# Performance work log

Hardware: AMD Instinct MI355X
Metric: run time of the kernel (lower is better)

## Reference

```python
import jax, jax.numpy as jnp
import numpy as np

N, E, C = 50000, 10000, 500
NNZ = 400000
IN_DIM, EDGE_DIM, NODE_DIM, COMP_DIM = 128, 128, 128, 128


def _glorot(key, shape):
    fan = shape[0] + shape[1]
    return jax.random.normal(key, shape, jnp.float32) * (2.0 / fan) ** 0.5


def _seg_mean(vals, idx, num):
    # mean aggregation over segments (scatter-add + count normalize)
    s = jax.ops.segment_sum(vals, idx, num_segments=num)
    cnt = jax.ops.segment_sum(jnp.ones((idx.shape[0], 1), vals.dtype), idx, num_segments=num)
    return s / jnp.maximum(cnt, 1.0)


def _prelu(v, a):
    return jnp.where(v >= 0, v, a * v)


def _conv(x, ni, ei, ec_e, ec_c, nc_n, nc_c, n_nodes, n_edges, n_comps,
          Wne, Wen, Wec, Wnc, a):
    # node -> hyperedge message passing
    e = _seg_mean((x @ Wne)[ni], ei, n_edges)            # [E, edge_dim]
    e_act = _prelu(e, a)
    # hyperedge -> node
    n = _seg_mean((e_act @ Wen)[ei], ni, n_nodes)        # [N, node_dim]
    # edge -> component and node -> component
    c = _seg_mean((e_act @ Wec)[ec_e], ec_c, n_comps) + \
        _seg_mean((x @ Wnc)[nc_n], nc_c, n_comps)        # [C, comp_dim]
    return n, e, c


def setup_inputs() -> dict:
    key = jax.random.key(0)
    ks = jax.random.split(key, 16)
    x = jax.random.normal(ks[0], (N, IN_DIM), jnp.float32)
    hyperedge_index = jnp.stack([
        jax.random.randint(ks[1], (NNZ,), 0, N),
        jax.random.randint(ks[2], (NNZ,), 0, E),
    ])
    hyperedge_component_index = jnp.stack([
        jnp.arange(E), jax.random.randint(ks[3], (E,), 0, C)])
    node_component_index = jnp.stack([
        jnp.arange(N), jax.random.randint(ks[4], (N,), 0, C)])
    return dict(
        x=x,
        hyperedge_index=hyperedge_index,
        hyperedge_component_index=hyperedge_component_index,
        node_component_index=node_component_index,
        num_nodes=N, num_edges=E, num_components=C,
        W_ne0=_glorot(ks[5], (IN_DIM, EDGE_DIM)),
        W_en0=_glorot(ks[6], (EDGE_DIM, NODE_DIM)),
        W_ec0=_glorot(ks[7], (EDGE_DIM, COMP_DIM)),
        W_nc0=_glorot(ks[8], (IN_DIM, COMP_DIM)),
        W_ne1=_glorot(ks[9], (NODE_DIM, EDGE_DIM)),
        W_en1=_glorot(ks[10], (EDGE_DIM, NODE_DIM)),
        W_ec1=_glorot(ks[11], (EDGE_DIM, COMP_DIM)),
        W_nc1=_glorot(ks[12], (NODE_DIM, COMP_DIM)),
        prelu_a=jnp.array(0.25, jnp.float32),
    )


def reference(x, hyperedge_index, hyperedge_component_index, node_component_index,
              num_nodes, num_edges, num_components,
              W_ne0, W_en0, W_ec0, W_nc0, W_ne1, W_en1, W_ec1, W_nc1, prelu_a):
    ni, ei = hyperedge_index[0], hyperedge_index[1]
    ec_e, ec_c = hyperedge_component_index[0], hyperedge_component_index[1]
    nc_n, nc_c = node_component_index[0], node_component_index[1]
    layers = [(W_ne0, W_en0, W_ec0, W_nc0), (W_ne1, W_en1, W_ec1, W_nc1)]
    e_out = c_out = None
    for Wne, Wen, Wec, Wnc in layers:
        n_out, e_out, c_out = _conv(x, ni, ei, ec_e, ec_c, nc_n, nc_c,
                                    num_nodes, num_edges, num_components,
                                    Wne, Wen, Wec, Wnc, prelu_a)
        x = _prelu(n_out, prelu_a)  # HyperEncoder applies act between/after layers
    return (x, e_out, c_out)
```

## Files before the change

kernel.cpp:

```cpp
#include <hip/hip_runtime.h>
#include <stdint.h>

typedef unsigned int u32;
typedef _Float16 f16;
typedef f16 half8 __attribute__((ext_vector_type(8)));
typedef float f32x4 __attribute__((ext_vector_type(4)));
#define TS 4096
#define KB2 256
#define CH 2048

__device__ __forceinline__ float bflo(u32 u) { return __uint_as_float(u << 16); }
__device__ __forceinline__ float bfhi(u32 u) { return __uint_as_float(u & 0xffff0000u); }
__device__ __forceinline__ u32 f2bf(float x) {
    u32 u = __float_as_uint(x);
    return (u + 0x7fffu + ((u >> 16) & 1u)) >> 16;
}
__device__ __forceinline__ u32 pack2(float a, float b) { return f2bf(a) | (f2bf(b) << 16); }

__device__ __forceinline__ int bstart2(int b, int total) {
    return (int)(((unsigned long long)b * (u32)total + KB2 - 1) / KB2);
}

__device__ __forceinline__ int blk_exscan(int v, int& total) {
    __shared__ int ws[5];
    int t = threadIdx.x, lane = t & 63, w = t >> 6;
    int inc = v;
    for (int d = 1; d < 64; d <<= 1) { int u = __shfl_up(inc, d, 64); if (lane >= d) inc += u; }
    __syncthreads();
    if (lane == 63) ws[w] = inc;
    __syncthreads();
    if (t == 0) { int acc = 0; for (int i = 0; i < 4; ++i) { int x = ws[i]; ws[i] = acc; acc += x; } ws[4] = acc; }
    __syncthreads();
    total = ws[4];
    return ws[w] + (inc - v);
}

__global__ void k_wprep(const float* __restrict__ W0, const float* __restrict__ W1,
                        const float* __restrict__ W2, const float* __restrict__ W3,
                        const float* __restrict__ W4, const float* __restrict__ W5,
                        f16* __restrict__ out) {
    int gid = blockIdx.x * 256 + threadIdx.x;
    if (gid >= 6 * 2048) return;
    int m = gid >> 11;
    int rem = gid & 2047;
    int c = rem >> 4;
    int s = rem & 15;
    const float* W = (m == 0) ? W0 : (m == 1) ? W1 : (m == 2) ? W2 :
                     (m == 3) ? W3 : (m == 4) ? W4 : W5;
    int khi = ((s & 7) ^ (c & 7)) | (s & 8);
    int k0 = khi << 3;
    union { f16 h[8]; uint4 v; } u;
#pragma unroll
    for (int j = 0; j < 8; ++j) u.h[j] = (f16)W[((k0 + j) << 7) + c];
    *(uint4*)(out + ((size_t)m << 14) + (c << 7) + (s << 3)) = u.v;
}

__global__ __launch_bounds__(256) void k_cvt_bhist(
        const float2* __restrict__ xin, u32* __restrict__ xout, int npairs,
        const int* __restrict__ ni, const int* __restrict__ ei,
        const int* __restrict__ nc_c, const int* __restrict__ ec_c,
        int* __restrict__ bcntE, int* __restrict__ bcntN,
        int* __restrict__ cnt_cn, int* __restrict__ cnt_ce,
        int nnz, int n, int e, int nbh) {
    int t = threadIdx.x;
    int b = blockIdx.x;
    if (b >= nbh) {
        int j = (b - nbh) * 256 + t;
        if (j < npairs) { float2 v = xin[j]; xout[j] = pack2(v.x, v.y); }
        return;
    }
    __shared__ int hE[KB2], hN[KB2];
    hE[t] = 0; hN[t] = 0;
    __syncthreads();
    int base = b * CH;
    int lim = base + CH; if (lim > nnz) lim = nnz;
    for (int i = base + t; i < lim; i += 256) {
        u32 v = (u32)ni[i], eg = (u32)ei[i];
        if (v >= (u32)n) v = 0;
        if (eg >= (u32)e) eg = 0;
        atomicAdd(&hE[(int)(((unsigned long long)eg * KB2) / (u32)e)], 1);
        atomicAdd(&hN[(int)(((unsigned long long)v  * KB2) / (u32)n)], 1);
    }
    __syncthreads();
    if (hE[t]) atomicAdd(&bcntE[t], hE[t]);
    if (hN[t]) atomicAdd(&bcntN[t], hN[t]);
    int gid = b * 256 + t, stride = nbh * 256;
    for (int j = gid; j < n + e; j += stride) {
        if (j < n) atomicAdd(&cnt_cn[nc_c[j]], 1);
        else       atomicAdd(&cnt_ce[ec_c[j - n]], 1);
    }
}

__global__ void k_cvt(const float2* __restrict__ in, u32* __restrict__ out, int npairs) {
    int j = blockIdx.x * blockDim.x + threadIdx.x;
    if (j < npairs) { float2 v = in[j]; out[j] = pack2(v.x, v.y); }
}

__global__ __launch_bounds__(256) void k_bscan(
        const int* __restrict__ bcntE, const int* __restrict__ bcntN,
        int* __restrict__ basesE, int* __restrict__ basesN,
        int* __restrict__ bcur_e, int* __restrict__ bcur_n,
        const int* __restrict__ cnt_cn, const int* __restrict__ cnt_ce,
        int* __restrict__ off_cn, int* __restrict__ off_ce,
        int* __restrict__ cur_cn, int* __restrict__ cur_ce, int c) {
    int t = threadIdx.x, tot;
    int v = bcntE[t];
    int ex = blk_exscan(v, tot);
    basesE[t] = ex; bcur_e[t] = ex;
    if (t == 0) basesE[KB2] = tot;
    v = bcntN[t];
    ex = blk_exscan(v, tot);
    basesN[t] = ex; bcur_n[t] = ex;
    if (t == 0) basesN[KB2] = tot;
    int i0 = 2 * t, i1 = 2 * t + 1;
    int v0 = (i0 < c) ? cnt_cn[i0] : 0;
    int v1 = (i1 < c) ? cnt_cn[i1] : 0;
    ex = blk_exscan(v0 + v1, tot);
    if (i0 < c) { off_cn[i0] = ex;      cur_cn[i0] = ex; }
    if (i1 < c) { off_cn[i1] = ex + v0; cur_cn[i1] = ex + v0; }
    if (t == 0) off_cn[c] = tot;
    v0 = (i0 < c) ? cnt_ce[i0] : 0;
    v1 = (i1 < c) ? cnt_ce[i1] : 0;
    ex = blk_exscan(v0 + v1, tot);
    if (i0 < c) { off_ce[i0] = ex;      cur_ce[i0] = ex; }
    if (i1 < c) { off_ce[i1] = ex + v0; cur_ce[i1] = ex + v0; }
    if (t == 0) off_ce[c] = tot;
}

__global__ __launch_bounds__(256) void k_part_a(
        const int* __restrict__ ni, const int* __restrict__ ei,
        int* __restrict__ bcur_e, int* __restrict__ bcur_n,
        u32* __restrict__ stg_e, u32* __restrict__ stg_n,
        const int* __restrict__ nc_n, const int* __restrict__ nc_c,
        const int* __restrict__ ec_e, const int* __restrict__ ec_c,
        int* __restrict__ cur_cn, int* __restrict__ cur_ce,
        int* __restrict__ csr_cn, int* __restrict__ csr_ce,
        int nnz, int n, int e) {
    __shared__ u32 pk[CH];
    __shared__ unsigned short bb[CH];
    __shared__ int hist[KB2];
    __shared__ int gb[KB2];
    int side = blockIdx.y;
    int base = blockIdx.x * CH;
    int cnt  = nnz - base; if (cnt > CH) cnt = CH;
    int t = threadIdx.x;
    for (int i = t; i < KB2; i += 256) hist[i] = 0;
    __syncthreads();
    u32 total = side ? (u32)n : (u32)e;
    for (int i = t; i < cnt; i += 256) {
        int v = ni[base + i], eg = ei[base + i];
        u32 key = side ? (u32)v : (u32)eg;
        u32 pay = side ? (u32)eg : (u32)v;
        if (key >= total) key = 0;
        u32 b = (u32)(((unsigned long long)key * KB2) / total);
        pk[i] = side ? (pay | (key << 14)) : (pay | (key << 16));
        bb[i] = (unsigned short)b;
        atomicAdd(&hist[b], 1);
    }
    __syncthreads();
    int* cursor = side ? bcur_n : bcur_e;
    u32* stg    = side ? stg_n  : stg_e;
    if (t < KB2) {
        int h = hist[t];
        gb[t] = h ? atomicAdd(&cursor[t], h) : 0;
        hist[t] = 0;
    }
    __syncthreads();
    for (int i = t; i < cnt; i += 256) {
        int b = bb[i];
        int r = atomicAdd(&hist[b], 1);
        stg[gb[b] + r] = pk[i];
    }
    int gid = blockIdx.x * 256 + t;
    int stride = gridDim.x * 256;
    if (side == 0) {
        for (int j = gid; j < e; j += stride) { int c = ec_c[j]; csr_ce[atomicAdd(&cur_ce[c], 1)] = ec_e[j]; }
    } else {
        for (int j = gid; j < n; j += stride) { int c = nc_c[j]; csr_cn[atomicAdd(&cur_cn[c], 1)] = nc_n[j]; }
    }
}

__global__ __launch_bounds__(256) void k_part_b2(
        const u32* __restrict__ stg_e, const u32* __restrict__ stg_n,
        const int* __restrict__ basesE, const int* __restrict__ basesN,
        int* __restrict__ off_e, int* __restrict__ off_n,
        int* __restrict__ csr_e, int* __restrict__ csr_n, int e, int n) {
    __shared__ int lcnt[256];
    int b = blockIdx.x, t = threadIdx.x;
    const u32* stg; const int* bases; int* off; int* csr; int total; int shift; u32 mask;
    if (b < KB2) { stg = stg_e; bases = basesE; off = off_e; csr = csr_e; total = e; shift = 16; mask = 0xFFFFu; }
    else { b -= KB2; stg = stg_n; bases = basesN; off = off_n; csr = csr_n; total = n; shift = 14; mask = 0x3FFFu; }
    int lo = bstart2(b, total), hi = bstart2(b + 1, total);
    int nid = hi - lo;
    int sbase = bases[b], send = bases[b + 1];
    lcnt[t] = 0;
    __syncthreads();
    for (int i = sbase + t; i < send; i += 256) {
        int key = (int)(stg[i] >> shift);
        atomicAdd(&lcnt[key - lo], 1);
    }
    __syncthreads();
    int cval = (t < nid) ? lcnt[t] : 0;
    int tot;
    int ex = blk_exscan(cval, tot);
    int cursor = sbase + ex;
    if (t < nid) { off[lo + t] = cursor; lcnt[t] = cursor; }
    if (t == 0 && hi == total) off[total] = send;
    __syncthreads();
    for (int i = sbase + t; i < send; i += 256) {
        u32 s = stg[i];
        int key = (int)(s >> shift);
        int pay = (int)(s & mask);
        int p = atomicAdd(&lcnt[key - lo], 1);
        csr[p] = pay;
    }
}

__global__ void k_hist_fb(const int* __restrict__ ni, const int* __restrict__ ei,
                          const int* __restrict__ nc_c, const int* __restrict__ ec_c,
                          int* __restrict__ deg_e, int* __restrict__ deg_n,
                          int* __restrict__ cnt_cn, int* __restrict__ cnt_ce,
                          int nnz, int n, int e) {
    int j = blockIdx.x * blockDim.x + threadIdx.x;
    if (j < nnz) {
        atomicAdd(&deg_e[ei[j]], 1);
        atomicAdd(&deg_n[ni[j]], 1);
    }
    if (j < n) atomicAdd(&cnt_cn[nc_c[j]], 1);
    if (j < e) atomicAdd(&cnt_ce[ec_c[j]], 1);
}

__device__ __forceinline__ void scan_sel(int b, int t0, int t01, int t012,
        const int* c0, int* o0, int* u0, int n0,
        const int* c1, int* o1, int* u1, int n1,
        const int* c2, int* o2, int* u2, int n2,
        const int* c3, int* o3, int* u3, int n3,
        const int*& cnt, int*& off, int*& cur, int& n, int& tile) {
    if (b < t0)        { cnt = c0; off = o0; cur = u0; n = n0; tile = b; }
    else if (b < t01)  { cnt = c1; off = o1; cur = u1; n = n1; tile = b - t0; }
    else if (b < t012) { cnt = c2; off = o2; cur = u2; n = n2; tile = b - t01; }
    else               { cnt = c3; off = o3; cur = u3; n = n3; tile = b - t012; }
}

__global__ void k_scan_p1(const int* c0, int n0, const int* c1, int n1,
                          const int* c2, int n2, const int* c3, int n3,
                          int t0, int t01, int t012, int* __restrict__ tilesum) {
    __shared__ int ws[4];
    int b = blockIdx.x;
    const int* cnt; int* off; int* cur; int n; int tile;
    scan_sel(b, t0, t01, t012, c0, nullptr, nullptr, n0, c1, nullptr, nullptr, n1,
             c2, nullptr, nullptr, n2, c3, nullptr, nullptr, n3, cnt, off, cur, n, tile);
    int base = tile * TS + threadIdx.x * 16;
    int s = 0;
#pragma unroll
    for (int i = 0; i < 16; ++i) { int idx = base + i; if (idx < n) s += cnt[idx]; }
    for (int d = 32; d; d >>= 1) s += __shfl_xor(s, d, 64);
    int lane = threadIdx.x & 63, w = threadIdx.x >> 6;
    if (lane == 0) ws[w] = s;
    __syncthreads();
    if (threadIdx.x == 0) tilesum[b] = ws[0] + ws[1] + ws[2] + ws[3];
}

__global__ void k_scan_p2(const int* __restrict__ tilesum, int* __restrict__ tilebase,
                          int t0, int t01, int t012, int t0123,
                          int* o0, int n0, int* o1, int n1, int* o2, int n2, int* o3, int n3) {
    if (threadIdx.x != 0 || blockIdx.x != 0) return;
    int carry = 0;
    for (int b = 0;    b < t0;    ++b) { tilebase[b] = carry; carry += tilesum[b]; } o0[n0] = carry;
    carry = 0;
    for (int b = t0;   b < t01;   ++b) { tilebase[b] = carry; carry += tilesum[b]; } o1[n1] = carry;
    carry = 0;
    for (int b = t01;  b < t012;  ++b) { tilebase[b] = carry; carry += tilesum[b]; } o2[n2] = carry;
    carry = 0;
    for (int b = t012; b < t0123; ++b) { tilebase[b] = carry; carry += tilesum[b]; } o3[n3] = carry;
}

__global__ void k_scan_p3(const int* c0, int* o0, int* u0, int n0,
                          const int* c1, int* o1, int* u1, int n1,
                          const int* c2, int* o2, int* u2, int n2,
                          const int* c3, int* o3, int* u3, int n3,
                          int t0, int t01, int t012, const int* __restrict__ tilebase) {
    __shared__ int wsum[4];
    int b = blockIdx.x;
    const int* cnt; int* off; int* cur; int n; int tile;
    scan_sel(b, t0, t01, t012, c0, o0, u0, n0, c1, o1, u1, n1,
             c2, o2, u2, n2, c3, o3, u3, n3, cnt, off, cur, n, tile);
    int lane = threadIdx.x & 63, w = threadIdx.x >> 6;
    int base = tile * TS + threadIdx.x * 16;
    int vals[16];
    int s = 0;
#pragma unroll
    for (int i = 0; i < 16; ++i) { int idx = base + i; int v = (idx < n) ? cnt[idx] : 0; vals[i] = v; s += v; }
    int inc = s;
    for (int d = 1; d < 64; d <<= 1) { int u = __shfl_up(inc, d, 64); if (lane >= d) inc += u; }
    if (lane == 63) wsum[w] = inc;
    __syncthreads();
    if (threadIdx.x == 0) {
        int acc = tilebase[b];
        for (int i = 0; i < 4; ++i) { int t = wsum[i]; wsum[i] = acc; acc += t; }
    }
    __syncthreads();
    int ex = wsum[w] + (inc - s);
#pragma unroll
    for (int i = 0; i < 16; ++i) {
        int idx = base + i;
        if (idx < n) { off[idx] = ex; cur[idx] = ex; }
        ex += vals[i];
    }
}

__global__ void k_scatter(const int* __restrict__ ni, const int* __restrict__ ei,
                          const int* __restrict__ nc_n, const int* __restrict__ nc_c,
                          const int* __restrict__ ec_e, const int* __restrict__ ec_c,
                          int* __restrict__ cur_e, int* __restrict__ cur_n,
                          int* __restrict__ cur_cn, int* __restrict__ cur_ce,
                          int* __restrict__ csr_e, int* __restrict__ csr_n,
                          int* __restrict__ csr_cn, int* __restrict__ csr_ce,
                          int nnz, int n, int e) {
    int j = blockIdx.x * blockDim.x + threadIdx.x;
    if (j < nnz) {
        int v = ni[j], eg = ei[j];
        csr_e[atomicAdd(&cur_e[eg], 1)] = v;
        csr_n[atomicAdd(&cur_n[v], 1)] = eg;
    }
    if (j < n) { int c = nc_c[j]; csr_cn[atomicAdd(&cur_cn[c], 1)] = nc_n[j]; }
    if (j < e) { int c = ec_c[j]; csr_ce[atomicAdd(&cur_ce[c], 1)] = ec_e[j]; }
}

__device__ __forceinline__ void agg4_body(const u32* __restrict__ in,
                                          const int* __restrict__ items,
                                          const int* __restrict__ off,
                                          float* __restrict__ out_f32,
                                          u32* __restrict__ out_bf,
                                          int nseg, int nrows, int do_prelu,
                                          const float* __restrict__ alpha_p, int seg) {
    int lane = threadIdx.x & 63;
    int rs = lane >> 4;
    int cc = lane & 15;
    if (seg >= nseg) return;
    int s0 = off[seg], s1 = off[seg + 1];
    const uint4* rows = (const uint4*)in;
    float a[8];
#pragma unroll
    for (int i = 0; i < 8; ++i) a[i] = 0.f;
    int base = s0;
    for (; base + 8 <= s1; base += 8) {
        u32 r0 = (u32)items[base + rs];
        u32 r1 = (u32)items[base + 4 + rs];
        r0 = (r0 < (u32)nrows) ? r0 : 0u;
        r1 = (r1 < (u32)nrows) ? r1 : 0u;
        uint4 v0 = rows[(size_t)r0 * 16 + cc];
        uint4 v1 = rows[(size_t)r1 * 16 + cc];
        a[0] += bflo(v0.x); a[1] += bfhi(v0.x); a[2] += bflo(v0.y); a[3] += bfhi(v0.y);
        a[4] += bflo(v0.z); a[5] += bfhi(v0.z); a[6] += bflo(v0.w); a[7] += bfhi(v0.w);
        a[0] += bflo(v1.x); a[1] += bfhi(v1.x); a[2] += bflo(v1.y); a[3] += bfhi(v1.y);
        a[4] += bflo(v1.z); a[5] += bfhi(v1.z); a[6] += bflo(v1.w); a[7] += bfhi(v1.w);
    }
    int idx = base + rs;
    if (idx < s1) {
        u32 r = (u32)items[idx]; r = (r < (u32)nrows) ? r : 0u;
        uint4 v = rows[(size_t)r * 16 + cc];
        a[0] += bflo(v.x); a[1] += bfhi(v.x); a[2] += bflo(v.y); a[3] += bfhi(v.y);
        a[4] += bflo(v.z); a[5] += bfhi(v.z); a[6] += bflo(v.w); a[7] += bfhi(v.w);
    }
    idx += 4;
    if (idx < s1) {
        u32 r = (u32)items[idx]; r = (r < (u32)nrows) ? r : 0u;
        uint4 v = rows[(size_t)r * 16 + cc];
        a[0] += bflo(v.x); a[1] += bfhi(v.x); a[2] += bflo(v.y); a[3] += bfhi(v.y);
        a[4] += bflo(v.z); a[5] += bfhi(v.z); a[6] += bflo(v.w); a[7] += bfhi(v.w);
    }
#pragma unroll
    for (int i = 0; i < 8; ++i) {
        a[i] += __shfl_xor(a[i], 16, 64);
        a[i] += __shfl_xor(a[i], 32, 64);
    }
    float inv = 1.f / fmaxf((float)(s1 - s0), 1.f);
#pragma unroll
    for (int i = 0; i < 8; ++i) a[i] *= inv;
    if (do_prelu) {
        float al = *alpha_p;
#pragma unroll
        for (int i = 0; i < 8; ++i) a[i] = (a[i] >= 0.f) ? a[i] : al * a[i];
    }
    if (rs == 0) {
        if (out_f32) {
            float* o = out_f32 + ((size_t)seg << 7) + cc * 8;
            *(float4*)o       = make_float4(a[0], a[1], a[2], a[3]);
            *(float4*)(o + 4) = make_float4(a[4], a[5], a[6], a[7]);
        }
        if (out_bf) {
            uint4 pk;
            pk.x = pack2(a[0], a[1]); pk.y = pack2(a[2], a[3]);
            pk.z = pack2(a[4], a[5]); pk.w = pack2(a[6], a[7]);
            *(uint4*)(out_bf + ((size_t)seg << 6) + cc * 4) = pk;
        }
    }
}

__global__ void k_agg4(const u32* __restrict__ in, const int* __restrict__ items,
                       const int* __restrict__ off, float* __restrict__ out_f32,
                       u32* __restrict__ out_bf,
                       int nseg, int nrows, int do_prelu, const float* __restrict__ alpha_p) {
    int seg = blockIdx.x * (blockDim.x >> 6) + (threadIdx.x >> 6);
    agg4_body(in, items, off, out_f32, out_bf, nseg, nrows, do_prelu, alpha_p, seg);
}

__global__ void k_agg_final(
        const u32* __restrict__ ybf, const int* __restrict__ csr_n, const int* __restrict__ off_n,
        float* __restrict__ out_x, int n, int e,
        const u32* __restrict__ eactbf, const int* __restrict__ csr_ce, const int* __restrict__ off_ce,
        float* __restrict__ ca_e,
        const u32* __restrict__ x1bf, const int* __restrict__ csr_cn, const int* __restrict__ off_cn,
        float* __restrict__ ca_n,
        int c, int nblkN, int ncb, const float* __restrict__ alpha_p) {
    int b = blockIdx.x;
    int wv = threadIdx.x >> 6;
    if (b < nblkN) {
        agg4_body(ybf, csr_n, off_n, out_x, nullptr, n, e, 1, alpha_p, b * 4 + wv);
    } else if (b < nblkN + ncb) {
        agg4_body(eactbf, csr_ce, off_ce, ca_e, nullptr, c, e, 0, nullptr, (b - nblkN) * 4 + wv);
    } else {
        agg4_body(x1bf, csr_cn, off_cn, ca_n, nullptr, c, n, 0, nullptr, (b - nblkN - ncb) * 4 + wv);
    }
}

__global__ __launch_bounds__(256) void k_mlp_mfma(
        const float* __restrict__ A,
        const f16* __restrict__ W1t, const f16* __restrict__ W2t,
        float* __restrict__ out_raw, u32* __restrict__ out_actbf,
        u32* __restrict__ out_ybf, int M, const float* __restrict__ alpha_p) {
    __shared__ f16 As[32 * 128];
    __shared__ f16 Wt[128 * 128];
    int t = threadIdx.x;
    int rb = blockIdx.x * 32;
    float al = *alpha_p;
    {
        const uint4* src = (const uint4*)W1t;
        uint4* dst = (uint4*)Wt;
        for (int i = t; i < 2048; i += 256) dst[i] = src[i];
    }
    for (int i = t; i < 32 * 32; i += 256) {
        int r = i >> 5, dc = i & 31;
        int row = rb + r;
        float4 v = make_float4(0.f, 0.f, 0.f, 0.f);
        if (row < M) v = *(const float4*)(A + ((size_t)row << 7) + dc * 4);
        f16* p = (f16*)((char*)As + (r << 8) + ((dc << 3) ^ ((r & 7) << 4)));
        p[0] = (f16)v.x; p[1] = (f16)v.y; p[2] = (f16)v.z; p[3] = (f16)v.w;
    }
    __syncthreads();

    int lane = t & 63, wv = t >> 6;
    int r0  = (wv >> 1) << 4;
    int ctb = (wv & 1) << 2;
    int frow = lane & 15;
    int fk = (lane >> 4) << 3;
    int rl0 = r0 + ((lane >> 4) << 2);
    int ar = r0 + frow;
    int asw = (ar & 7) << 4;

    f32x4 acc[4] = {{0.f,0.f,0.f,0.f},{0.f,0.f,0.f,0.f},{0.f,0.f,0.f,0.f},{0.f,0.f,0.f,0.f}};
#pragma unroll
    for (int ks = 0; ks < 4; ++ks) {
        int kb2 = (ks * 32 + fk) << 1;
        half8 a = *(const half8*)((const char*)As + (ar << 8) + (kb2 ^ asw));
#pragma unroll
        for (int j = 0; j < 4; ++j) {
            int c = ((ctb + j) << 4) + frow;
            half8 b = *(const half8*)((const char*)Wt + (c << 8) + (kb2 ^ ((c & 7) << 4)));
            acc[j] = __builtin_amdgcn_mfma_f32_16x16x32_f16(a, b, acc[j], 0, 0, 0);
        }
    }
    __syncthreads();
    {
        const uint4* src = (const uint4*)W2t;
        uint4* dst = (uint4*)Wt;
        for (int i = t; i < 2048; i += 256) dst[i] = src[i];
    }
#pragma unroll
    for (int j = 0; j < 4; ++j) {
        int c = ((ctb + j) << 4) + frow;
#pragma unroll
        for (int rg = 0; rg < 4; ++rg) {
            int rl = rl0 + rg;
            int row = rb + rl;
            float ev = acc[j][rg];
            if (out_raw != nullptr && row < M) out_raw[((size_t)row << 7) + c] = ev;
            float av = (ev >= 0.f) ? ev : al * ev;
            float po = __shfl_xor(av, 1, 64);
            if (out_actbf != nullptr && (frow & 1) == 0 && row < M)
                out_actbf[((size_t)row << 6) + (c >> 1)] = pack2(av, po);
            *(f16*)((char*)As + (rl << 8) + (((c << 1)) ^ ((rl & 7) << 4))) = (f16)av;
        }
    }
    __syncthreads();
    f32x4 acc2[4] = {{0.f,0.f,0.f,0.f},{0.f,0.f,0.f,0.f},{0.f,0.f,0.f,0.f},{0.f,0.f,0.f,0.f}};
#pragma unroll
    for (int ks = 0; ks < 4; ++ks) {
        int kb2 = (ks * 32 + fk) << 1;
        half8 a = *(const half8*)((const char*)As + (ar << 8) + (kb2 ^ asw));
#pragma unroll
        for (int j = 0; j < 4; ++j) {
            int c = ((ctb + j) << 4) + frow;
            half8 b = *(const half8*)((const char*)Wt + (c << 8) + (kb2 ^ ((c & 7) << 4)));
            acc2[j] = __builtin_amdgcn_mfma_f32_16x16x32_f16(a, b, acc2[j], 0, 0, 0);
        }
    }
#pragma unroll
    for (int j = 0; j < 4; ++j) {
        int c = ((ctb + j) << 4) + frow;
#pragma unroll
        for (int rg = 0; rg < 4; ++rg) {
            int rl = rl0 + rg;
            int row = rb + rl;
            float yv = acc2[j][rg];
            float po = __shfl_xor(yv, 1, 64);
            if ((frow & 1) == 0 && row < M)
                out_ybf[((size_t)row << 6) + (c >> 1)] = pack2(yv, po);
        }
    }
}

__global__ __launch_bounds__(256) void k_gemm_mfma(
        const float* __restrict__ A1, const f16* __restrict__ W1t,
        const float* __restrict__ A2, const f16* __restrict__ W2t,
        float* __restrict__ out, int M) {
    __shared__ f16 Asd[2][32 * 128];
    __shared__ f16 Wt[128 * 128];
    int t = threadIdx.x;
    int rb = blockIdx.x * 32;
    {
        const uint4* src = (const uint4*)W1t;
        uint4* dst = (uint4*)Wt;
        for (int i = t; i < 2048; i += 256) dst[i] = src[i];
    }
    for (int p = 0; p < 2; ++p) {
        const float* Ap = p ? A2 : A1;
        for (int i = t; i < 32 * 32; i += 256) {
            int r = i >> 5, dc = i & 31;
            int row = rb + r;
            float4 v = make_float4(0.f, 0.f, 0.f, 0.f);
            if (row < M) v = *(const float4*)(Ap + ((size_t)row << 7) + dc * 4);
            f16* q = (f16*)((char*)Asd[p] + (r << 8) + ((dc << 3) ^ ((r & 7) << 4)));
            q[0] = (f16)v.x; q[1] = (f16)v.y; q[2] = (f16)v.z; q[3] = (f16)v.w;
        }
    }
    __syncthreads();

    int lane = t & 63, wv = t >> 6;
    int r0  = (wv >> 1) << 4;
    int ctb = (wv & 1) << 2;
    int frow = lane & 15;
    int fk = (lane >> 4) << 3;
    int rl0 = r0 + ((lane >> 4) << 2);
    int ar = r0 + frow;
    int asw = (ar & 7) << 4;

    f32x4 acc[4] = {{0.f,0.f,0.f,0.f},{0.f,0.f,0.f,0.f},{0.f,0.f,0.f,0.f},{0.f,0.f,0.f,0.f}};
#pragma unroll
    for (int ks = 0; ks < 4; ++ks) {
        int kb2 = (ks * 32 + fk) << 1;
        half8 a = *(const half8*)((const char*)Asd[0] + (ar << 8) + (kb2 ^ asw));
#pragma unroll
        for (int j = 0; j < 4; ++j) {
            int c = ((ctb + j) << 4) + frow;
            half8 b = *(const half8*)((const char*)Wt + (c << 8) + (kb2 ^ ((c & 7) << 4)));
            acc[j] = __builtin_amdgcn_mfma_f32_16x16x32_f16(a, b, acc[j], 0, 0, 0);
        }
    }
    __syncthreads();
    {
        const uint4* src = (const uint4*)W2t;
        uint4* dst = (uint4*)Wt;
        for (int i = t; i < 2048; i += 256) dst[i] = src[i];
    }
    __syncthreads();
#pragma unroll
    for (int ks = 0; ks < 4; ++ks) {
        int kb2 = (ks * 32 + fk) << 1;
        half8 a = *(const half8*)((const char*)Asd[1] + (ar << 8) + (kb2 ^ asw));
#pragma unroll
        for (int j = 0; j < 4; ++j) {
            int c = ((ctb + j) << 4) + frow;
            half8 b = *(const half8*)((const char*)Wt + (c << 8) + (kb2 ^ ((c & 7) << 4)));
            acc[j] = __builtin_amdgcn_mfma_f32_16x16x32_f16(a, b, acc[j], 0, 0, 0);
        }
    }
#pragma unroll
    for (int j = 0; j < 4; ++j) {
        int c = ((ctb + j) << 4) + frow;
#pragma unroll
        for (int rg = 0; rg < 4; ++rg) {
            int row = rb + rl0 + rg;
            if (row < M) out[((size_t)row << 7) + c] = acc[j][rg];
        }
    }
}

extern "C" void kernel_launch(void* const* d_in, const int* in_sizes, int n_in,
                              void* d_out, int out_size, void* d_ws, size_t ws_size,
                              hipStream_t stream) {
    const int N   = in_sizes[0] / 128;
    const int NNZ = in_sizes[1] / 2;
    const int E   = in_sizes[2] / 2;
    const int C   = 500;

    const float* x0 = (const float*)d_in[0];
    const int* ni   = (const int*)d_in[1];
    const int* ei   = ni + NNZ;
    const int* ec_e = (const int*)d_in[2];
    const int* ec_c = ec_e + E;
    const int* nc_n = (const int*)d_in[3];
    const int* nc_c = nc_n + N;
    const float* Wne0 = (const float*)d_in[7];
    const float* Wen0 = (const float*)d_in[8];
    const float* Wne1 = (const float*)d_in[11];
    const float* Wen1 = (const float*)d_in[12];
    const float* Wec1 = (const float*)d_in[13];
    const float* Wnc1 = (const float*)d_in[14];
    const float* alpha = (const float*)d_in[15];

    float* out_x = (float*)d_out;
    float* out_e = out_x + (size_t)N * 128;
    float* out_c = out_e + (size_t)E * 128;

    char* w = (char*)d_ws;
    auto alloc = [&](size_t bytes) { char* p = w; w += (bytes + 255) & ~(size_t)255; return p; };
    int* zgrp   = (int*)alloc((size_t)(2 * KB2 + 2 * C) * 4);
    int* bcntE  = zgrp;
    int* bcntN  = zgrp + KB2;
    int* cnt_cn = zgrp + 2 * KB2;
    int* cnt_ce = zgrp + 2 * KB2 + C;
    int* off_e  = (int*)alloc((size_t)(E + 1) * 4);
    int* off_n  = (int*)alloc((size_t)(N + 1) * 4);
    int* off_cn = (int*)alloc((size_t)(C + 1) * 4);
    int* off_ce = (int*)alloc((size_t)(C + 1) * 4);
    int* cur_cn = (int*)alloc((size_t)C * 4);
    int* cur_ce = (int*)alloc((size_t)C * 4);
    int* csr_e  = (int*)alloc((size_t)NNZ * 4);
    int* csr_n  = (int*)alloc((size_t)NNZ * 4);
    int* csr_cn = (int*)alloc((size_t)N * 4);
    int* csr_ce = (int*)alloc((size_t)E * 4);
    int* basesE = (int*)alloc((size_t)(KB2 + 1) * 4);
    int* basesN = (int*)alloc((size_t)(KB2 + 1) * 4);
    int* bcur_e = (int*)alloc(KB2 * 4);
    int* bcur_n = (int*)alloc(KB2 * 4);
    u32* stg_e  = (u32*)alloc((size_t)NNZ * 4);
    u32* stg_n  = (u32*)alloc((size_t)NNZ * 4);
    u32* xbf    = (u32*)alloc((size_t)N * 64 * 4);
    u32* x1bf   = (u32*)alloc((size_t)N * 64 * 4);
    u32* ybf    = (u32*)alloc((size_t)E * 64 * 4);
    u32* eactbf = (u32*)alloc((size_t)E * 64 * 4);
    float* xa   = (float*)alloc((size_t)E * 128 * 4);
    float* ca_e = (float*)alloc((size_t)C * 128 * 4);
    float* ca_n = (float*)alloc((size_t)C * 128 * 4);
    f16* wt6    = (f16*)alloc((size_t)6 * 16384 * 2);
    int* deg_e    = (int*)alloc((size_t)E * 4);
    int* deg_n    = (int*)alloc((size_t)N * 4);
    int* cur_e    = (int*)alloc((size_t)E * 4);
    int* cur_n    = (int*)alloc((size_t)N * 4);
    int* tilesum  = (int*)alloc(64 * 4);
    int* tilebase = (int*)alloc(64 * 4);

    const int th = 256;
    const int npairs = N * 64;
    const int nbh = (NNZ + CH - 1) / CH;

    hipMemsetAsync(zgrp, 0, (size_t)(2 * KB2 + 2 * C) * 4, stream);
    k_wprep<<<48, 256, 0, stream>>>(Wne0, Wen0, Wne1, Wen1, Wec1, Wnc1, wt6);

    bool binned = (E <= 16384) && (N <= 65536) && (E >= KB2) && (N >= KB2) &&
                  ((N + KB2 - 1) / KB2 <= 256) && (C <= 512);
    if (binned) {
        const int nkc = (npairs + th - 1) / th;
        k_cvt_bhist<<<nbh + nkc, 256, 0, stream>>>((const float2*)x0, xbf, npairs,
                                                   ni, ei, nc_c, ec_c,
                                                   bcntE, bcntN, cnt_cn, cnt_ce, NNZ, N, E, nbh);
        k_bscan<<<1, 256, 0, stream>>>(bcntE, bcntN, basesE, basesN, bcur_e, bcur_n,
                                       cnt_cn, cnt_ce, off_cn, off_ce, cur_cn, cur_ce, C);
        {
            dim3 ga(nbh, 2);
            k_part_a<<<ga, 256, 0, stream>>>(ni, ei, bcur_e, bcur_n, stg_e, stg_n,
                                             nc_n, nc_c, ec_e, ec_c,
                                             cur_cn, cur_ce, csr_cn, csr_ce, NNZ, N, E);
        }
        k_part_b2<<<2 * KB2, 256, 0, stream>>>(stg_e, stg_n, basesE, basesN,
                                               off_e, off_n, csr_e, csr_n, E, N);
    } else {
        hipMemsetAsync(deg_e, 0, (size_t)E * 4, stream);
        hipMemsetAsync(deg_n, 0, (size_t)N * 4, stream);
        k_cvt<<<(npairs + th - 1) / th, th, 0, stream>>>((const float2*)x0, xbf, npairs);
        k_hist_fb<<<(NNZ > N + E ? NNZ : N + E) / th + 1, th, 0, stream>>>(
            ni, ei, nc_c, ec_c, deg_e, deg_n, cnt_cn, cnt_ce, NNZ, N, E);
        const int t0 = (E + TS - 1) / TS, t1 = (N + TS - 1) / TS;
        const int t2 = (C + TS - 1) / TS, t3 = (C + TS - 1) / TS;
        const int t01 = t0 + t1, t012 = t01 + t2, t0123 = t012 + t3;
        k_scan_p1<<<t0123, 256, 0, stream>>>(deg_e, E, deg_n, N, cnt_cn, C, cnt_ce, C,
                                             t0, t01, t012, tilesum);
        k_scan_p2<<<1, 64, 0, stream>>>(tilesum, tilebase, t0, t01, t012, t0123,
                                        off_e, E, off_n, N, off_cn, C, off_ce, C);
        k_scan_p3<<<t0123, 256, 0, stream>>>(deg_e, off_e, cur_e, E,
                                             deg_n, off_n, cur_n, N,
                                             cnt_cn, off_cn, cur_cn, C,
                                             cnt_ce, off_ce, cur_ce, C,
                                             t0, t01, t012, tilebase);
        k_scatter<<<(NNZ + th - 1) / th, th, 0, stream>>>(ni, ei, nc_n, nc_c, ec_e, ec_c,
                                                          cur_e, cur_n, cur_cn, cur_ce,
                                                          csr_e, csr_n, csr_cn, csr_ce, NNZ, N, E);
    }

    const int gmlp = (E + 31) / 32;
    k_agg4<<<(E + 3) / 4, 256, 0, stream>>>(xbf, csr_e, off_e, xa, nullptr, E, N, 0, alpha);
    k_mlp_mfma<<<gmlp, 256, 0, stream>>>(xa, wt6, wt6 + 16384, nullptr, nullptr, ybf, E, alpha);
    k_agg4<<<(N + 3) / 4, 256, 0, stream>>>(ybf, csr_n, off_n, nullptr, x1bf, N, E, 1, alpha);
    k_agg4<<<(E + 3) / 4, 256, 0, stream>>>(x1bf, csr_e, off_e, xa, nullptr, E, N, 0, alpha);
    k_mlp_mfma<<<gmlp, 256, 0, stream>>>(xa, wt6 + 2 * 16384, wt6 + 3 * 16384,
                                         out_e, eactbf, ybf, E, alpha);
    {
        const int nblkN = (N + 3) / 4;
        const int ncb   = (C + 3) / 4;
        k_agg_final<<<nblkN + 2 * ncb, 256, 0, stream>>>(
            ybf, csr_n, off_n, out_x, N, E,
            eactbf, csr_ce, off_ce, ca_e,
            x1bf,   csr_cn, off_cn, ca_n,
            C, nblkN, ncb, alpha);
    }
    k_gemm_mfma<<<(C + 31) / 32, 256, 0, stream>>>(ca_e, wt6 + 4 * 16384,
                                                   ca_n, wt6 + 5 * 16384, out_c, C);
}
```

Baseline: 268.9 us.

## Fuse edge aggregation into MLP kernel and merge front-end prep kernels

Edge-side segment-mean aggregation now runs inside the MFMA MLP kernel. It writes mean rows straight into shared memory as fp16 instead of going through an fp32 global buffer `xa`. The weight prep, conversion/histogram and block scan kernels are merged into a single launch, with the last-block ticket pattern doing the scan. The gather loop is also unrolled to 16 items. This removes several launches and a global round trip, at the cost of less parallelism in the aggregation phase (each wave handles 8 segments serially) and higher register and shared-memory pressure.

```diff
diff --git a/kernel.cpp b/kernel.cpp
--- a/kernel.cpp
+++ b/kernel.cpp
@@ -35,41 +35,144 @@
     return ws[w] + (inc - v);
 }
 
-__global__ void k_wprep(const float* __restrict__ W0, const float* __restrict__ W1,
-                        const float* __restrict__ W2, const float* __restrict__ W3,
-                        const float* __restrict__ W4, const float* __restrict__ W5,
-                        f16* __restrict__ out) {
-    int gid = blockIdx.x * 256 + threadIdx.x;
-    if (gid >= 6 * 2048) return;
-    int m = gid >> 11;
-    int rem = gid & 2047;
-    int c = rem >> 4;
-    int s = rem & 15;
-    const float* W = (m == 0) ? W0 : (m == 1) ? W1 : (m == 2) ? W2 :
-                     (m == 3) ? W3 : (m == 4) ? W4 : W5;
-    int khi = ((s & 7) ^ (c & 7)) | (s & 8);
-    int k0 = khi << 3;
-    union { f16 h[8]; uint4 v; } u;
-#pragma unroll
-    for (int j = 0; j < 8; ++j) u.h[j] = (f16)W[((k0 + j) << 7) + c];
-    *(uint4*)(out + ((size_t)m << 14) + (c << 7) + (s << 3)) = u.v;
-}
-
-__global__ __launch_bounds__(256) void k_cvt_bhist(
+#define ACC8(v) do { \
+    a[0] += bflo((v).x); a[1] += bfhi((v).x); a[2] += bflo((v).y); a[3] += bfhi((v).y); \
+    a[4] += bflo((v).z); a[5] += bfhi((v).z); a[6] += bflo((v).w); a[7] += bfhi((v).w); } while (0)
+
+__device__ __forceinline__ void seg_mean8(const u32* __restrict__ in,
+                                          const int* __restrict__ items,
+                                          const int* __restrict__ off,
+                                          int nseg, int nrows, int seg, float a[8]) {
+    int lane = threadIdx.x & 63;
+    int rs = lane >> 4;
+    int cc = lane & 15;
+#pragma unroll
+    for (int i = 0; i < 8; ++i) a[i] = 0.f;
+    int s0 = 0, s1 = 0;
+    if (seg < nseg) { s0 = off[seg]; s1 = off[seg + 1]; }
+    const uint4* rows = (const uint4*)in;
+    int base = s0;
+    for (; base + 16 <= s1; base += 16) {
+        u32 r0 = (u32)items[base + rs];
+        u32 r1 = (u32)items[base + 4 + rs];
+        u32 r2 = (u32)items[base + 8 + rs];
+        u32 r3 = (u32)items[base + 12 + rs];
+        r0 = (r0 < (u32)nrows) ? r0 : 0u;
+        r1 = (r1 < (u32)nrows) ? r1 : 0u;
+        r2 = (r2 < (u32)nrows) ? r2 : 0u;
+        r3 = (r3 < (u32)nrows) ? r3 : 0u;
+        uint4 v0 = rows[(size_t)r0 * 16 + cc];
+        uint4 v1 = rows[(size_t)r1 * 16 + cc];
+        uint4 v2 = rows[(size_t)r2 * 16 + cc];
+        uint4 v3 = rows[(size_t)r3 * 16 + cc];
+        ACC8(v0); ACC8(v1); ACC8(v2); ACC8(v3);
+    }
+    for (; base + 8 <= s1; base += 8) {
+        u32 r0 = (u32)items[base + rs];
+        u32 r1 = (u32)items[base + 4 + rs];
+        r0 = (r0 < (u32)nrows) ? r0 : 0u;
+        r1 = (r1 < (u32)nrows) ? r1 : 0u;
+        uint4 v0 = rows[(size_t)r0 * 16 + cc];
+        uint4 v1 = rows[(size_t)r1 * 16 + cc];
+        ACC8(v0); ACC8(v1);
+    }
+    int idx = base + rs;
+    if (idx < s1) {
+        u32 r = (u32)items[idx]; r = (r < (u32)nrows) ? r : 0u;
+        uint4 v = rows[(size_t)r * 16 + cc];
+        ACC8(v);
+    }
+    idx += 4;
+    if (idx < s1) {
+        u32 r = (u32)items[idx]; r = (r < (u32)nrows) ? r : 0u;
+        uint4 v = rows[(size_t)r * 16 + cc];
+        ACC8(v);
+    }
+#pragma unroll
+    for (int i = 0; i < 8; ++i) {
+        a[i] += __shfl_xor(a[i], 16, 64);
+        a[i] += __shfl_xor(a[i], 32, 64);
+    }
+    float inv = 1.f / fmaxf((float)(s1 - s0), 1.f);
+#pragma unroll
+    for (int i = 0; i < 8; ++i) a[i] *= inv;
+}
+
+__device__ __forceinline__ void agg4_body(const u32* __restrict__ in,
+                                          const int* __restrict__ items,
+                                          const int* __restrict__ off,
+                                          float* __restrict__ out_f32,
+                                          u32* __restrict__ out_bf,
+                                          int nseg, int nrows, int do_prelu,
+                                          const float* __restrict__ alpha_p, int seg) {
+    if (seg >= nseg) return;
+    int lane = threadIdx.x & 63;
+    int rs = lane >> 4;
+    int cc = lane & 15;
+    float a[8];
+    seg_mean8(in, items, off, nseg, nrows, seg, a);
+    if (do_prelu) {
+        float al = *alpha_p;
+#pragma unroll
+        for (int i = 0; i < 8; ++i) a[i] = (a[i] >= 0.f) ? a[i] : al * a[i];
+    }
+    if (rs == 0) {
+        if (out_f32) {
+            float* o = out_f32 + ((size_t)seg << 7) + cc * 8;
+            *(float4*)o       = make_float4(a[0], a[1], a[2], a[3]);
+            *(float4*)(o + 4) = make_float4(a[4], a[5], a[6], a[7]);
+        }
+        if (out_bf) {
+            uint4 pk;
+            pk.x = pack2(a[0], a[1]); pk.y = pack2(a[2], a[3]);
+            pk.z = pack2(a[4], a[5]); pk.w = pack2(a[6], a[7]);
+            *(uint4*)(out_bf + ((size_t)seg << 6) + cc * 4) = pk;
+        }
+    }
+}
+
+__global__ __launch_bounds__(256) void k_front(
         const float2* __restrict__ xin, u32* __restrict__ xout, int npairs,
         const int* __restrict__ ni, const int* __restrict__ ei,
         const int* __restrict__ nc_c, const int* __restrict__ ec_c,
         int* __restrict__ bcntE, int* __restrict__ bcntN,
         int* __restrict__ cnt_cn, int* __restrict__ cnt_ce,
-        int nnz, int n, int e, int nbh) {
+        int nnz, int n, int e, int nbh, int nkc,
+        int* __restrict__ ticket,
+        int* __restrict__ basesE, int* __restrict__ basesN,
+        int* __restrict__ bcur_e, int* __restrict__ bcur_n,
+        int* __restrict__ off_cn, int* __restrict__ off_ce,
+        int* __restrict__ cur_cn, int* __restrict__ cur_ce, int c,
+        const float* __restrict__ W0, const float* __restrict__ W1,
+        const float* __restrict__ W2, const float* __restrict__ W3,
+        const float* __restrict__ W4, const float* __restrict__ W5,
+        f16* __restrict__ wt6) {
     int t = threadIdx.x;
     int b = blockIdx.x;
+    if (b >= nbh + nkc) {
+        int gid = (b - nbh - nkc) * 256 + t;
+        if (gid >= 6 * 2048) return;
+        int m = gid >> 11;
+        int rem = gid & 2047;
+        int cq = rem >> 4;
+        int s = rem & 15;
+        const float* W = (m == 0) ? W0 : (m == 1) ? W1 : (m == 2) ? W2 :
+                         (m == 3) ? W3 : (m == 4) ? W4 : W5;
+        int khi = ((s & 7) ^ (cq & 7)) | (s & 8);
+        int k0 = khi << 3;
+        union { f16 h[8]; uint4 v; } u;
+#pragma unroll
+        for (int j = 0; j < 8; ++j) u.h[j] = (f16)W[((k0 + j) << 7) + cq];
+        *(uint4*)(wt6 + ((size_t)m << 14) + (cq << 7) + (s << 3)) = u.v;
+        return;
+    }
     if (b >= nbh) {
         int j = (b - nbh) * 256 + t;
         if (j < npairs) { float2 v = xin[j]; xout[j] = pack2(v.x, v.y); }
         return;
     }
     __shared__ int hE[KB2], hN[KB2];
+    __shared__ int lastflag;
     hE[t] = 0; hN[t] = 0;
     __syncthreads();
     int base = b * CH;
@@ -89,21 +192,15 @@
         if (j < n) atomicAdd(&cnt_cn[nc_c[j]], 1);
         else       atomicAdd(&cnt_ce[ec_c[j - n]], 1);
     }
-}
-
-__global__ void k_cvt(const float2* __restrict__ in, u32* __restrict__ out, int npairs) {
-    int j = blockIdx.x * blockDim.x + threadIdx.x;
-    if (j < npairs) { float2 v = in[j]; out[j] = pack2(v.x, v.y); }
-}
-
-__global__ __launch_bounds__(256) void k_bscan(
-        const int* __restrict__ bcntE, const int* __restrict__ bcntN,
-        int* __restrict__ basesE, int* __restrict__ basesN,
-        int* __restrict__ bcur_e, int* __restrict__ bcur_n,
-        const int* __restrict__ cnt_cn, const int* __restrict__ cnt_ce,
-        int* __restrict__ off_cn, int* __restrict__ off_ce,
-        int* __restrict__ cur_cn, int* __restrict__ cur_ce, int c) {
-    int t = threadIdx.x, tot;
+    __syncthreads();
+    if (t == 0) {
+        __threadfence();
+        lastflag = (atomicAdd(ticket, 1) == nbh - 1);
+    }
+    __syncthreads();
+    if (!lastflag) return;
+    __threadfence();
+    int tot;
     int v = bcntE[t];
     int ex = blk_exscan(v, tot);
     basesE[t] = ex; bcur_e[t] = ex;
@@ -327,86 +424,16 @@
     if (j < e) { int c = ec_c[j]; csr_ce[atomicAdd(&cur_ce[c], 1)] = ec_e[j]; }
 }
 
-__device__ __forceinline__ void agg4_body(const u32* __restrict__ in,
-                                          const int* __restrict__ items,
-                                          const int* __restrict__ off,
-                                          float* __restrict__ out_f32,
-                                          u32* __restrict__ out_bf,
-                                          int nseg, int nrows, int do_prelu,
-                                          const float* __restrict__ alpha_p, int seg) {
-    int lane = threadIdx.x & 63;
-    int rs = lane >> 4;
-    int cc = lane & 15;
-    if (seg >= nseg) return;
-    int s0 = off[seg], s1 = off[seg + 1];
-    const uint4* rows = (const uint4*)in;
-    float a[8];
-#pragma unroll
-    for (int i = 0; i < 8; ++i) a[i] = 0.f;
-    int base = s0;
-    for (; base + 8 <= s1; base += 8) {
-        u32 r0 = (u32)items[base + rs];
-        u32 r1 = (u32)items[base + 4 + rs];
-        r0 = (r0 < (u32)nrows) ? r0 : 0u;
-        r1 = (r1 < (u32)nrows) ? r1 : 0u;
-        uint4 v0 = rows[(size_t)r0 * 16 + cc];
-        uint4 v1 = rows[(size_t)r1 * 16 + cc];
-        a[0] += bflo(v0.x); a[1] += bfhi(v0.x); a[2] += bflo(v0.y); a[3] += bfhi(v0.y);
-        a[4] += bflo(v0.z); a[5] += bfhi(v0.z); a[6] += bflo(v0.w); a[7] += bfhi(v0.w);
-        a[0] += bflo(v1.x); a[1] += bfhi(v1.x); a[2] += bflo(v1.y); a[3] += bfhi(v1.y);
-        a[4] += bflo(v1.z); a[5] += bfhi(v1.z); a[6] += bflo(v1.w); a[7] += bfhi(v1.w);
-    }
-    int idx = base + rs;
-    if (idx < s1) {
-        u32 r = (u32)items[idx]; r = (r < (u32)nrows) ? r : 0u;
-        uint4 v = rows[(size_t)r * 16 + cc];
-        a[0] += bflo(v.x); a[1] += bfhi(v.x); a[2] += bflo(v.y); a[3] += bfhi(v.y);
-        a[4] += bflo(v.z); a[5] += bfhi(v.z); a[6] += bflo(v.w); a[7] += bfhi(v.w);
-    }
-    idx += 4;
-    if (idx < s1) {
-        u32 r = (u32)items[idx]; r = (r < (u32)nrows) ? r : 0u;
-        uint4 v = rows[(size_t)r * 16 + cc];
-        a[0] += bflo(v.x); a[1] += bfhi(v.x); a[2] += bflo(v.y); a[3] += bfhi(v.y);
-        a[4] += bflo(v.z); a[5] += bfhi(v.z); a[6] += bflo(v.w); a[7] += bfhi(v.w);
-    }
-#pragma unroll
-    for (int i = 0; i < 8; ++i) {
-        a[i] += __shfl_xor(a[i], 16, 64);
-        a[i] += __shfl_xor(a[i], 32, 64);
-    }
-    float inv = 1.f / fmaxf((float)(s1 - s0), 1.f);
-#pragma unroll
-    for (int i = 0; i < 8; ++i) a[i] *= inv;
-    if (do_prelu) {
-        float al = *alpha_p;
-#pragma unroll
-        for (int i = 0; i < 8; ++i) a[i] = (a[i] >= 0.f) ? a[i] : al * a[i];
-    }
-    if (rs == 0) {
-        if (out_f32) {
-            float* o = out_f32 + ((size_t)seg << 7) + cc * 8;
-            *(float4*)o       = make_float4(a[0], a[1], a[2], a[3]);
-            *(float4*)(o + 4) = make_float4(a[4], a[5], a[6], a[7]);
-        }
-        if (out_bf) {
-            uint4 pk;
-            pk.x = pack2(a[0], a[1]); pk.y = pack2(a[2], a[3]);
-            pk.z = pack2(a[4], a[5]); pk.w = pack2(a[6], a[7]);
-            *(uint4*)(out_bf + ((size_t)seg << 6) + cc * 4) = pk;
-        }
-    }
-}
-
-__global__ void k_agg4(const u32* __restrict__ in, const int* __restrict__ items,
-                       const int* __restrict__ off, float* __restrict__ out_f32,
-                       u32* __restrict__ out_bf,
-                       int nseg, int nrows, int do_prelu, const float* __restrict__ alpha_p) {
+__global__ __launch_bounds__(256) void k_agg4(
+        const u32* __restrict__ in, const int* __restrict__ items,
+        const int* __restrict__ off, float* __restrict__ out_f32,
+        u32* __restrict__ out_bf,
+        int nseg, int nrows, int do_prelu, const float* __restrict__ alpha_p) {
     int seg = blockIdx.x * (blockDim.x >> 6) + (threadIdx.x >> 6);
     agg4_body(in, items, off, out_f32, out_bf, nseg, nrows, do_prelu, alpha_p, seg);
 }
 
-__global__ void k_agg_final(
+__global__ __launch_bounds__(256) void k_agg_final(
         const u32* __restrict__ ybf, const int* __restrict__ csr_n, const int* __restrict__ off_n,
         float* __restrict__ out_x, int n, int e,
         const u32* __restrict__ eactbf, const int* __restrict__ csr_ce, const int* __restrict__ off_ce,
@@ -425,14 +452,15 @@
     }
 }
 
-__global__ __launch_bounds__(256) void k_mlp_mfma(
-        const float* __restrict__ A,
+__global__ __launch_bounds__(256) void k_aggmlp(
+        const u32* __restrict__ gin, const int* __restrict__ items,
+        const int* __restrict__ off, int nseg, int nrows,
         const f16* __restrict__ W1t, const f16* __restrict__ W2t,
         float* __restrict__ out_raw, u32* __restrict__ out_actbf,
-        u32* __restrict__ out_ybf, int M, const float* __restrict__ alpha_p) {
+        u32* __restrict__ out_ybf, const float* __restrict__ alpha_p) {
     __shared__ f16 As[32 * 128];
     __shared__ f16 Wt[128 * 128];
-    int t = threadIdx.x;
+    int t = threadIdx.x, lane = t & 63, wv = t >> 6;
     int rb = blockIdx.x * 32;
     float al = *alpha_p;
     {
@@ -440,23 +468,27 @@
         uint4* dst = (uint4*)Wt;
         for (int i = t; i < 2048; i += 256) dst[i] = src[i];
     }
-    for (int i = t; i < 32 * 32; i += 256) {
-        int r = i >> 5, dc = i & 31;
-        int row = rb + r;
-        float4 v = make_float4(0.f, 0.f, 0.f, 0.f);
-        if (row < M) v = *(const float4*)(A + ((size_t)row << 7) + dc * 4);
-        f16* p = (f16*)((char*)As + (r << 8) + ((dc << 3) ^ ((r & 7) << 4)));
-        p[0] = (f16)v.x; p[1] = (f16)v.y; p[2] = (f16)v.z; p[3] = (f16)v.w;
-    }
-    __syncthreads();
-
-    int lane = t & 63, wv = t >> 6;
-    int r0  = (wv >> 1) << 4;
+    int rs = lane >> 4, cc = lane & 15;
+#pragma unroll 1
+    for (int s = 0; s < 8; ++s) {
+        int rl = wv * 8 + s;
+        float a[8];
+        seg_mean8(gin, items, off, nseg, nrows, rb + rl, a);
+        if (rs == 0) {
+            union { f16 h[8]; uint4 v; } u;
+#pragma unroll
+            for (int i = 0; i < 8; ++i) u.h[i] = (f16)a[i];
+            *(uint4*)((char*)As + (rl << 8) + ((cc << 4) ^ ((rl & 7) << 4))) = u.v;
+        }
+    }
+    __syncthreads();
+
+    int r0q = (wv >> 1) << 4;
     int ctb = (wv & 1) << 2;
     int frow = lane & 15;
     int fk = (lane >> 4) << 3;
-    int rl0 = r0 + ((lane >> 4) << 2);
-    int ar = r0 + frow;
+    int rl0 = r0q + ((lane >> 4) << 2);
+    int ar = r0q + frow;
     int asw = (ar & 7) << 4;
 
     f32x4 acc[4] = {{0.f,0.f,0.f,0.f},{0.f,0.f,0.f,0.f},{0.f,0.f,0.f,0.f},{0.f,0.f,0.f,0.f}};
@@ -485,10 +517,10 @@
             int rl = rl0 + rg;
             int row = rb + rl;
             float ev = acc[j][rg];
-            if (out_raw != nullptr && row < M) out_raw[((size_t)row << 7) + c] = ev;
+            if (out_raw != nullptr && row < nseg) out_raw[((size_t)row << 7) + c] = ev;
             float av = (ev >= 0.f) ? ev : al * ev;
             float po = __shfl_xor(av, 1, 64);
-            if (out_actbf != nullptr && (frow & 1) == 0 && row < M)
+            if (out_actbf != nullptr && (frow & 1) == 0 && row < nseg)
                 out_actbf[((size_t)row << 6) + (c >> 1)] = pack2(av, po);
             *(f16*)((char*)As + (rl << 8) + (((c << 1)) ^ ((rl & 7) << 4))) = (f16)av;
         }
@@ -515,7 +547,7 @@
             int row = rb + rl;
             float yv = acc2[j][rg];
             float po = __shfl_xor(yv, 1, 64);
-            if ((frow & 1) == 0 && row < M)
+            if ((frow & 1) == 0 && row < nseg)
                 out_ybf[((size_t)row << 6) + (c >> 1)] = pack2(yv, po);
         }
     }
@@ -626,11 +658,12 @@
 
     char* w = (char*)d_ws;
     auto alloc = [&](size_t bytes) { char* p = w; w += (bytes + 255) & ~(size_t)255; return p; };
-    int* zgrp   = (int*)alloc((size_t)(2 * KB2 + 2 * C) * 4);
+    int* zgrp   = (int*)alloc((size_t)(2 * KB2 + 2 * C + 1) * 4);
     int* bcntE  = zgrp;
     int* bcntN  = zgrp + KB2;
     int* cnt_cn = zgrp + 2 * KB2;
     int* cnt_ce = zgrp + 2 * KB2 + C;
+    int* ticket = zgrp + 2 * KB2 + 2 * C;
     int* off_e  = (int*)alloc((size_t)(E + 1) * 4);
     int* off_n  = (int*)alloc((size_t)(N + 1) * 4);
     int* off_cn = (int*)alloc((size_t)(C + 1) * 4);
@@ -651,7 +684,6 @@
     u32* x1bf   = (u32*)alloc((size_t)N * 64 * 4);
     u32* ybf    = (u32*)alloc((size_t)E * 64 * 4);
     u32* eactbf = (u32*)alloc((size_t)E * 64 * 4);
-    float* xa   = (float*)alloc((size_t)E * 128 * 4);
     float* ca_e = (float*)alloc((size_t)C * 128 * 4);
     float* ca_n = (float*)alloc((size_t)C * 128 * 4);
     f16* wt6    = (f16*)alloc((size_t)6 * 16384 * 2);
@@ -665,19 +697,21 @@
     const int th = 256;
     const int npairs = N * 64;
     const int nbh = (NNZ + CH - 1) / CH;
-
-    hipMemsetAsync(zgrp, 0, (size_t)(2 * KB2 + 2 * C) * 4, stream);
-    k_wprep<<<48, 256, 0, stream>>>(Wne0, Wen0, Wne1, Wen1, Wec1, Wnc1, wt6);
+    const int nkc = (npairs + th - 1) / th;
 
     bool binned = (E <= 16384) && (N <= 65536) && (E >= KB2) && (N >= KB2) &&
                   ((N + KB2 - 1) / KB2 <= 256) && (C <= 512);
+    const int nbh_eff = binned ? nbh : 0;
+
+    hipMemsetAsync(zgrp, 0, (size_t)(2 * KB2 + 2 * C + 1) * 4, stream);
+    k_front<<<nbh_eff + nkc + 48, 256, 0, stream>>>(
+        (const float2*)x0, xbf, npairs, ni, ei, nc_c, ec_c,
+        bcntE, bcntN, cnt_cn, cnt_ce, NNZ, N, E, nbh_eff, nkc,
+        ticket, basesE, basesN, bcur_e, bcur_n,
+        off_cn, off_ce, cur_cn, cur_ce, C,
+        Wne0, Wen0, Wne1, Wen1, Wec1, Wnc1, wt6);
+
     if (binned) {
-        const int nkc = (npairs + th - 1) / th;
-        k_cvt_bhist<<<nbh + nkc, 256, 0, stream>>>((const float2*)x0, xbf, npairs,
-                                                   ni, ei, nc_c, ec_c,
-                                                   bcntE, bcntN, cnt_cn, cnt_ce, NNZ, N, E, nbh);
-        k_bscan<<<1, 256, 0, stream>>>(bcntE, bcntN, basesE, basesN, bcur_e, bcur_n,
-                                       cnt_cn, cnt_ce, off_cn, off_ce, cur_cn, cur_ce, C);
         {
             dim3 ga(nbh, 2);
             k_part_a<<<ga, 256, 0, stream>>>(ni, ei, bcur_e, bcur_n, stg_e, stg_n,
@@ -689,7 +723,6 @@
     } else {
         hipMemsetAsync(deg_e, 0, (size_t)E * 4, stream);
         hipMemsetAsync(deg_n, 0, (size_t)N * 4, stream);
-        k_cvt<<<(npairs + th - 1) / th, th, 0, stream>>>((const float2*)x0, xbf, npairs);
         k_hist_fb<<<(NNZ > N + E ? NNZ : N + E) / th + 1, th, 0, stream>>>(
             ni, ei, nc_c, ec_c, deg_e, deg_n, cnt_cn, cnt_ce, NNZ, N, E);
         const int t0 = (E + TS - 1) / TS, t1 = (N + TS - 1) / TS;
@@ -710,12 +743,12 @@
     }
 
     const int gmlp = (E + 31) / 32;
-    k_agg4<<<(E + 3) / 4, 256, 0, stream>>>(xbf, csr_e, off_e, xa, nullptr, E, N, 0, alpha);
-    k_mlp_mfma<<<gmlp, 256, 0, stream>>>(xa, wt6, wt6 + 16384, nullptr, nullptr, ybf, E, alpha);
+    k_aggmlp<<<gmlp, 256, 0, stream>>>(xbf, csr_e, off_e, E, N,
+                                       wt6, wt6 + 16384, nullptr, nullptr, ybf, alpha);
     k_agg4<<<(N + 3) / 4, 256, 0, stream>>>(ybf, csr_n, off_n, nullptr, x1bf, N, E, 1, alpha);
-    k_agg4<<<(E + 3) / 4, 256, 0, stream>>>(x1bf, csr_e, off_e, xa, nullptr, E, N, 0, alpha);
-    k_mlp_mfma<<<gmlp, 256, 0, stream>>>(xa, wt6 + 2 * 16384, wt6 + 3 * 16384,
-                                         out_e, eactbf, ybf, E, alpha);
+    k_aggmlp<<<gmlp, 256, 0, stream>>>(x1bf, csr_e, off_e, E, N,
+                                       wt6 + 2 * 16384, wt6 + 3 * 16384,
+                                       out_e, eactbf, ybf, alpha);
     {
         const int nblkN = (N + 3) / 4;
         const int ncb   = (C + 3) / 4;
```

Result: slower. 285.0 us (+6.0%).
